# Kernel optimization log

Measured on AMD Instinct MI355X. Metric: run time of the kernel, lower is better.

## Reference

```python
import jax, jax.numpy as jnp
import numpy as np

B, S, T, K = 96, 4, 16, 36           # groups, fixed 4 slots, max tags per slot, num boxes
V_DIM, Q_DIM, H = 1024, 512, 512


def setup_inputs() -> dict:
    key = jax.random.key(0)
    k_v, k_q, k_m, k_w1, k_b1, k_w2, k_b2 = jax.random.split(key, 7)

    # deterministic ragged lengths in [1, T], cyclic -> sum is exact
    lengths = (np.arange(B * S) % T) + 1              # [B*S], sum = 24 * 136 = 3264
    N = int(lengths.sum())                            # total rows in v / q
    # binary tag-attention mask: first `len` positions set per slot
    tags_attention = (np.arange(T)[None, :] < lengths[:, None]).astype(np.int32)
    tags_attention = jnp.asarray(tags_attention.reshape(B, S, T))

    v = jax.random.normal(k_v, (N, K, V_DIM), dtype=jnp.float32)
    q = jax.random.normal(k_q, (N, Q_DIM), dtype=jnp.float32)

    # box mask: random 0/1 but guarantee at least one valid box per group
    box_mask = (jax.random.uniform(k_m, (B, K)) < 0.9).astype(jnp.float32)
    box_mask = box_mask.at[:, 0].set(1.0)

    # FCNet (weight-normed Linear + ReLU; dropout inactive at eval) and scoring Linear
    w1 = jax.random.normal(k_w1, (V_DIM + Q_DIM, H), dtype=jnp.float32) * 0.02
    b1 = jax.random.normal(k_b1, (H,), dtype=jnp.float32) * 0.02
    w2 = jax.random.normal(k_w2, (H,), dtype=jnp.float32) * 0.02
    b2 = jax.random.normal(k_b2, (), dtype=jnp.float32) * 0.02

    return {"v": v, "q": q, "box_mask": box_mask, "tags_attention": tags_attention,
            "w1": w1, "b1": b1, "w2": w2, "b2": b2}


def reference(v, q, box_mask, tags_attention, w1, b1, w2, b2):
    N, Kb, _ = v.shape
    # logits: concat(v, q repeated over boxes) -> ReLU FC -> scalar score per box
    vq = jnp.concatenate([v, jnp.broadcast_to(q[:, None, :], (N, Kb, q.shape[-1]))], axis=-1)
    joint = jax.nn.relu(jnp.einsum('nkd,dh->nkh', vq, w1) + b1)      # [N, K, H]
    logits = jnp.einsum('nkh,h->nk', joint, w2) + b2                 # [N, K]

    # pad_sequence: ragged rows -> [B, S, T, K] via vectorized gather
    Bg, Sg, Tg = tags_attention.shape
    lengths = tags_attention.sum(-1).reshape(-1)                     # [B*S]
    starts = jnp.cumsum(lengths) - lengths                           # exclusive cumsum
    idx = starts[:, None] + jnp.arange(Tg)                           # [B*S, T]
    valid = jnp.arange(Tg)[None, :] < lengths[:, None]               # [B*S, T]
    gathered = jnp.take(logits, jnp.clip(idx, 0, N - 1), axis=0)     # [B*S, T, K]
    padded = jnp.where(valid[..., None], gathered, 0.0).reshape(Bg, Sg, Tg, Kb)

    # masked_softmax (allennlp-style) over the box dim with box_mask [B,1,1,K]
    mask = box_mask[:, None, None, :]
    s = jax.nn.softmax(padded * mask, axis=-1) * mask
    w = s / (s.sum(axis=-1, keepdims=True) + 1e-13)
    return w
```

## Files before the change

kernel.cpp:

```cpp
#include <hip/hip_runtime.h>
#include <hip/hip_bf16.h>
#include <cstdint>
#include <cstddef>

#define BB 96
#define SS 4
#define TT 16
#define KK 36
#define VDIM 1024
#define QDIM 512
#define HH 512
#define W1R 1536
#define NROWS 3264
#define MM (NROWS * KK)

typedef __attribute__((ext_vector_type(8))) short short8;
typedef __attribute__((ext_vector_type(4))) float f32x4;

static __device__ __forceinline__ unsigned short f2bf(float f) {
    union { float f; unsigned u; } v; v.f = f;
    unsigned u = v.u;
    u += 0x7FFFu + ((u >> 16) & 1u);
    return (unsigned short)(u >> 16);
}

static __device__ __forceinline__ unsigned pk2(float lo, float hi) {
    __hip_bfloat162 h = __float22bfloat162_rn(make_float2(lo, hi));
    union { __hip_bfloat162 h; unsigned u; } cv;
    cv.h = h;
    return cv.u;
}

__device__ __forceinline__ void gload_lds16(const void* g, void* l) {
    __builtin_amdgcn_global_load_lds(
        (const __attribute__((address_space(1))) unsigned int*)g,
        (__attribute__((address_space(3))) unsigned int*)l, 16, 0, 0);
}

#define SB() __builtin_amdgcn_sched_barrier(0)

__global__ __launch_bounds__(256) void prep_w1T(const float* __restrict__ w1,
                                                unsigned short* __restrict__ w1T) {
    int k = blockIdx.x * 256 + threadIdx.x;
    int c = blockIdx.y;
    w1T[(size_t)c * W1R + k] = f2bf(w1[(size_t)k * HH + c]);
}

__global__ __launch_bounds__(512) void starts_kernel(const int* __restrict__ tags,
                                                     int* __restrict__ starts,
                                                     int* __restrict__ lengths) {
    __shared__ int sl[BB * SS];
    int tid = threadIdx.x;
    int len = 0;
    if (tid < BB * SS) {
#pragma unroll
        for (int i = 0; i < TT; ++i) len += tags[tid * TT + i];
        sl[tid] = len;
    }
    __syncthreads();
    for (int off = 1; off < BB * SS; off <<= 1) {
        int v = 0;
        if (tid < BB * SS && tid >= off) v = sl[tid - off];
        __syncthreads();
        if (tid < BB * SS) sl[tid] += v;
        __syncthreads();
    }
    if (tid < BB * SS) { starts[tid] = sl[tid] - len; lengths[tid] = len; }
}

__global__ __launch_bounds__(256, 3) void qproj_mfma(const float* __restrict__ q,
                                                     const unsigned short* __restrict__ w1T,
                                                     const float* __restrict__ b1,
                                                     float* __restrict__ qp) {
    __shared__ __align__(16) unsigned short At[2][64 * 64];
    __shared__ __align__(16) unsigned short Bt[2][128 * 64];

    int tid = threadIdx.x, lane = tid & 63, wid = tid >> 6;
    int wm = wid >> 1, wn = wid & 1;
    int bx = blockIdx.x;
    int nb = bx & 3, mb = bx >> 2;
    int n0q = mb * 64, cb = nb * 128;
    int lr = lane & 15, lg = lane >> 4;

    const float* a_base = q + (size_t)(n0q + wid * 16 + (lane >> 4)) * QDIM + (lane & 15) * 4;
    const unsigned short* b_base = w1T + (size_t)(cb + wid * 32 + (lane >> 3)) * W1R + 1024
                                 + (((lane & 7) ^ (lane >> 3)) * 8);

    f32x4 acc[2][4];
#pragma unroll
    for (int mt = 0; mt < 2; ++mt)
#pragma unroll
        for (int nt = 0; nt < 4; ++nt) acc[mt][nt] = (f32x4){0.f, 0.f, 0.f, 0.f};

#define QP_CVT_WRITE(DST, AR)                                                  \
    _Pragma("unroll") for (int p = 0; p < 4; ++p) {                            \
        int r = wid * 16 + (lane >> 4) + p * 4;                                \
        int boff = r * 128 + ((((lane & 15) * 8)) ^ ((r & 7) << 4));           \
        uint2 d;                                                               \
        d.x = pk2(AR[p].x, AR[p].y);                                           \
        d.y = pk2(AR[p].z, AR[p].w);                                           \
        *(uint2*)((char*)(DST) + boff) = d;                                    \
    }

#define QP_COMPUTE(AC, BC)                                                     \
    _Pragma("unroll") for (int kk = 0; kk < 2; ++kk) {                         \
        short8 af[2], bf[4];                                                   \
        _Pragma("unroll") for (int mt = 0; mt < 2; ++mt) {                     \
            int R = wm * 32 + mt * 16 + lr;                                    \
            int off = R * 128 + ((kk * 64 + lg * 16) ^ ((R & 7) << 4));        \
            af[mt] = *(const short8*)((const char*)(AC) + off);                \
        }                                                                      \
        _Pragma("unroll") for (int nt = 0; nt < 4; ++nt) {                     \
            int R = wn * 64 + nt * 16 + lr;                                    \
            int off = R * 128 + ((kk * 64 + lg * 16) ^ ((R & 7) << 4));        \
            bf[nt] = *(const short8*)((const char*)(BC) + off);                \
        }                                                                      \
        __builtin_amdgcn_s_setprio(1);                                         \
        _Pragma("unroll") for (int mt = 0; mt < 2; ++mt)                       \
            _Pragma("unroll") for (int nt = 0; nt < 4; ++nt)                   \
                acc[mt][nt] = __builtin_amdgcn_mfma_f32_16x16x32_bf16(         \
                    af[mt], bf[nt], acc[mt][nt], 0, 0, 0);                     \
        __builtin_amdgcn_s_setprio(0);                                         \
    }

    {
        float4 ar[4];
#pragma unroll
        for (int p = 0; p < 4; ++p) ar[p] = *(const float4*)(a_base + (size_t)p * 4 * QDIM);
#pragma unroll
        for (int o = 0; o < 4; ++o)
            gload_lds16(b_base + (size_t)o * 8 * W1R, &Bt[0][(wid * 32 + o * 8) * 64]);
        SB();
        QP_CVT_WRITE(&At[0][0], ar)
    }
#pragma unroll 1
    for (int t = 0; t < 7; ++t) {
        int k0 = (t + 1) * 64;
        const unsigned short* Ac = &At[t & 1][0];
        const unsigned short* Bc = &Bt[t & 1][0];
        unsigned short* An = &At[(t + 1) & 1][0];
        unsigned short* Bn = &Bt[(t + 1) & 1][0];
        float4 ar[4];
#pragma unroll
        for (int p = 0; p < 4; ++p)
            ar[p] = *(const float4*)(a_base + (size_t)p * 4 * QDIM + k0);
#pragma unroll
        for (int o = 0; o < 4; ++o)
            gload_lds16(b_base + (size_t)o * 8 * W1R + k0, &Bn[(wid * 32 + o * 8) * 64]);
        SB();
        asm volatile("s_waitcnt vmcnt(8)" ::: "memory");
        asm volatile("s_waitcnt lgkmcnt(0)" ::: "memory");
        __builtin_amdgcn_s_barrier();
        SB();
        QP_COMPUTE(Ac, Bc)
        SB();
        QP_CVT_WRITE(An, ar)
    }
    SB();
    asm volatile("s_waitcnt vmcnt(0)" ::: "memory");
    asm volatile("s_waitcnt lgkmcnt(0)" ::: "memory");
    __builtin_amdgcn_s_barrier();
    SB();
    QP_COMPUTE(&At[1][0], &Bt[1][0])
#undef QP_COMPUTE
#undef QP_CVT_WRITE

#pragma unroll
    for (int nt = 0; nt < 4; ++nt) {
        int c = cb + wn * 64 + nt * 16 + lr;
        float b1v = b1[c];
#pragma unroll
        for (int mt = 0; mt < 2; ++mt)
#pragma unroll
            for (int r = 0; r < 4; ++r) {
                int row = wm * 32 + mt * 16 + lg * 4 + r;
                qp[(size_t)(n0q + row) * HH + c] = acc[mt][nt][r] + b1v;
            }
    }
}

__global__ __launch_bounds__(256, 3) void main_gemm(const float* __restrict__ v,
                                                    const unsigned short* __restrict__ w1T,
                                                    const float* __restrict__ qp,
                                                    const float* __restrict__ w2,
                                                    float* __restrict__ logits4) {
    __shared__ __align__(16) unsigned short At[128 * 64];
    __shared__ __align__(16) unsigned short Bt[2][128 * 64];

    int tid = threadIdx.x, lane = tid & 63, wid = tid >> 6;
    int wm = wid >> 1, wn = wid & 1;
    int bx = blockIdx.x;
    int orig = (bx & 7) * 459 + (bx >> 3);
    int nb = orig & 3, mb = orig >> 2;
    int m0 = mb * 128, cb = nb * 128;
    int lr = lane & 15, lg = lane >> 4;

    const float* a_base = v + (size_t)(m0 + wid * 32 + (lane >> 4)) * VDIM + (lane & 15) * 4;
    const unsigned short* b_base = w1T + (size_t)(cb + wid * 32 + (lane >> 3)) * W1R
                                 + (((lane & 7) ^ (lane >> 3)) * 8);

    f32x4 acc[4][4];
#pragma unroll
    for (int mt = 0; mt < 4; ++mt)
#pragma unroll
        for (int nt = 0; nt < 4; ++nt) acc[mt][nt] = (f32x4){0.f, 0.f, 0.f, 0.f};

#define MG_CVT_WRITE(AR)                                                       \
    _Pragma("unroll") for (int p = 0; p < 8; ++p) {                            \
        int r = wid * 32 + (lane >> 4) + p * 4;                                \
        int boff = r * 128 + ((((lane & 15) * 8)) ^ ((r & 7) << 4));           \
        uint2 d;                                                               \
        d.x = pk2(AR[p].x, AR[p].y);                                           \
        d.y = pk2(AR[p].z, AR[p].w);                                           \
        *(uint2*)((char*)&At[0] + boff) = d;                                   \
    }

#define MG_READ_A(AF, KKC)                                                     \
    _Pragma("unroll") for (int mt = 0; mt < 4; ++mt) {                         \
        int R = wm * 64 + mt * 16 + lr;                                        \
        int off = R * 128 + (((KKC) * 64 + lg * 16) ^ ((R & 7) << 4));         \
        AF[mt] = *(const short8*)((const char*)&At[0] + off);                  \
    }

#define MG_READ_B(BF, BC, KKC)                                                 \
    _Pragma("unroll") for (int nt = 0; nt < 4; ++nt) {                         \
        int R = wn * 64 + nt * 16 + lr;                                        \
        int off = R * 128 + (((KKC) * 64 + lg * 16) ^ ((R & 7) << 4));         \
        BF[nt] = *(const short8*)((const char*)(BC) + off);                    \
    }

#define MG_MFMA(AF, BF)                                                        \
    __builtin_amdgcn_s_setprio(1);                                             \
    _Pragma("unroll") for (int mt = 0; mt < 4; ++mt)                           \
        _Pragma("unroll") for (int nt = 0; nt < 4; ++nt)                       \
            acc[mt][nt] = __builtin_amdgcn_mfma_f32_16x16x32_bf16(             \
                AF[mt], BF[nt], acc[mt][nt], 0, 0, 0);                         \
    __builtin_amdgcn_s_setprio(0);

    {
#pragma unroll
        for (int o = 0; o < 4; ++o)
            gload_lds16(b_base + (size_t)o * 8 * W1R, &Bt[0][(wid * 32 + o * 8) * 64]);
        float4 ar[8];
#pragma unroll
        for (int p = 0; p < 8; ++p) ar[p] = *(const float4*)(a_base + (size_t)p * 4 * VDIM);
        SB();
        MG_CVT_WRITE(ar)
    }

#pragma unroll 1
    for (int t = 0; t < 16; ++t) {
        int kA = (t < 15) ? (t + 1) * 64 : 960;
        const unsigned short* Bc = &Bt[t & 1][0];
        unsigned short* Bn = &Bt[(t + 1) & 1][0];
        float4 ar[8];
#pragma unroll
        for (int p = 0; p < 8; ++p)
            ar[p] = *(const float4*)(a_base + (size_t)p * 4 * VDIM + kA);
        SB();
        asm volatile("s_waitcnt vmcnt(8)" ::: "memory");
        asm volatile("s_waitcnt lgkmcnt(0)" ::: "memory");
        __builtin_amdgcn_s_barrier();
        SB();
        if (t < 15) {
#pragma unroll
            for (int o = 0; o < 4; ++o)
                gload_lds16(b_base + (size_t)o * 8 * W1R + kA, Bn + (wid * 32 + o * 8) * 64);
        }
        SB();
        {
            short8 af0[4], bf0[4];
            MG_READ_A(af0, 0)
            MG_READ_B(bf0, Bc, 0)
            MG_MFMA(af0, bf0)
        }
        {
            short8 af1[4], bf1[4];
            MG_READ_A(af1, 1)
            MG_READ_B(bf1, Bc, 1)
            MG_MFMA(af1, bf1)
        }
        SB();
        asm volatile("s_waitcnt lgkmcnt(0)" ::: "memory");
        __builtin_amdgcn_s_barrier();
        SB();
        if (t < 15) { MG_CVT_WRITE(ar) }
    }
#undef MG_MFMA
#undef MG_READ_A
#undef MG_READ_B
#undef MG_CVT_WRITE

    __syncthreads();
    float* qs = (float*)&At[0];
    float* fl = qs + 5 * 128;
    int n0 = m0 / KK;
    for (int i = tid; i < 5 * 128; i += 256) {
        int nn = n0 + (i >> 7);
        if (nn >= NROWS) nn = NROWS - 1;
        qs[i] = qp[(size_t)nn * HH + cb + (i & 127)];
    }
    __syncthreads();

    float part[4][4] = {{0.f}};
#pragma unroll
    for (int nt = 0; nt < 4; ++nt) {
        int c = wn * 64 + nt * 16 + lr;
        float w2v = w2[cb + c];
#pragma unroll
        for (int mt = 0; mt < 4; ++mt)
#pragma unroll
            for (int r = 0; r < 4; ++r) {
                int row = wm * 64 + mt * 16 + lg * 4 + r;
                int ni = (m0 + row) / KK - n0;
                float pre = acc[mt][nt][r] + qs[ni * 128 + c];
                part[mt][r] += fmaxf(pre, 0.f) * w2v;
            }
    }
#pragma unroll
    for (int mt = 0; mt < 4; ++mt)
#pragma unroll
        for (int r = 0; r < 4; ++r) {
            float s = part[mt][r];
            s += __shfl_xor(s, 1, 64);
            s += __shfl_xor(s, 2, 64);
            s += __shfl_xor(s, 4, 64);
            s += __shfl_xor(s, 8, 64);
            if (lr == 0) fl[wn * 128 + wm * 64 + mt * 16 + lg * 4 + r] = s;
        }
    __syncthreads();
    if (tid < 128)
        logits4[(size_t)nb * MM + m0 + tid] = fl[tid] + fl[128 + tid];
}

__global__ __launch_bounds__(256) void softmax_kernel(const float* __restrict__ logits4,
                                                      const float* __restrict__ box_mask,
                                                      const int* __restrict__ starts,
                                                      const int* __restrict__ lengths,
                                                      float* __restrict__ out) {
    int lane = threadIdx.x & 63;
    int g = blockIdx.x * 4 + (threadIdx.x >> 6);
    int t   = g & (TT - 1);
    int row = g >> 4;
    int b   = row >> 2;

    int length = lengths[row];
    int start  = starts[row];

    int k = lane;
    bool kv = k < KK;
    float mval = kv ? box_mask[b * KK + k] : 0.f;
    bool act = kv && (mval != 0.f);

    float l = 0.f;
    if (act && t < length) {
        size_t idx = (size_t)(start + t) * KK + k;
        l = logits4[idx] + logits4[MM + idx] + logits4[2 * (size_t)MM + idx]
          + logits4[3 * (size_t)MM + idx];
    }

    float lm = act ? l : -1e30f;
#pragma unroll
    for (int off = 32; off >= 1; off >>= 1) lm = fmaxf(lm, __shfl_xor(lm, off, 64));

    float e = act ? expf(l - lm) : 0.f;
    float se = e;
#pragma unroll
    for (int off = 32; off >= 1; off >>= 1) se += __shfl_xor(se, off, 64);

    if (kv) out[(size_t)g * KK + k] = e / se;
}

extern "C" void kernel_launch(void* const* d_in, const int* in_sizes, int n_in,
                              void* d_out, int out_size, void* d_ws, size_t ws_size,
                              hipStream_t stream) {
    const float* v        = (const float*)d_in[0];
    const float* q        = (const float*)d_in[1];
    const float* box_mask = (const float*)d_in[2];
    const int*   tags     = (const int*)d_in[3];
    const float* w1       = (const float*)d_in[4];
    const float* b1       = (const float*)d_in[5];
    const float* w2       = (const float*)d_in[6];

    char* ws = (char*)d_ws;
    unsigned short* w1T   = (unsigned short*)ws;
    float* qp      = (float*)(ws + 1572864);
    float* logits4 = (float*)(ws + 1572864 + 6684672);
    int*   starts  = (int*)(ws + 1572864 + 6684672 + 1880064);
    int*   lengths = (int*)(ws + 1572864 + 6684672 + 1880064 + 1536);
    float* out     = (float*)d_out;

    hipLaunchKernelGGL(prep_w1T, dim3(6, 512), dim3(256), 0, stream, w1, w1T);
    hipLaunchKernelGGL(starts_kernel, dim3(1), dim3(512), 0, stream, tags, starts, lengths);
    hipLaunchKernelGGL(qproj_mfma, dim3((NROWS / 64) * 4), dim3(256), 0, stream,
                       q, w1T, b1, qp);
    hipLaunchKernelGGL(main_gemm, dim3((MM / 128) * 4), dim3(256), 0, stream,
                       v, w1T, qp, w2, logits4);
    hipLaunchKernelGGL(softmax_kernel, dim3((BB * SS * TT) / 4), dim3(256), 0, stream,
                       logits4, box_mask, starts, lengths, out);
}
```

Measured before the change: 233.2 us.

## Widen main GEMM tile to 128x256 with 512-thread blocks

Changes the main fused GEMM block tile from 128x128 with 4 waves to 128x256 with 8 waves, so each block covers half of H instead of a quarter. Each converted fp32 A tile of v is reused across twice as many output columns, halving the number of times v is read from global memory and converted to bf16. The B buffer in LDS grows, the partial-logit buffer shrinks from four slices to two, and the softmax kernel sums two partials. XCD-aware block remapping is adjusted for the new grid size. Larger blocks may reduce occupancy and raise LDS pressure.

```diff
diff --git a/kernel.cpp b/kernel.cpp
--- a/kernel.cpp
+++ b/kernel.cpp
@@ -179,23 +179,25 @@
     }
 }
 
-__global__ __launch_bounds__(256, 3) void main_gemm(const float* __restrict__ v,
+__global__ __launch_bounds__(512, 4) void main_gemm(const float* __restrict__ v,
                                                     const unsigned short* __restrict__ w1T,
                                                     const float* __restrict__ qp,
                                                     const float* __restrict__ w2,
-                                                    float* __restrict__ logits4) {
+                                                    float* __restrict__ logits2) {
     __shared__ __align__(16) unsigned short At[128 * 64];
-    __shared__ __align__(16) unsigned short Bt[2][128 * 64];
+    __shared__ __align__(16) unsigned short Bt[2][256 * 64];
 
     int tid = threadIdx.x, lane = tid & 63, wid = tid >> 6;
-    int wm = wid >> 1, wn = wid & 1;
+    int wm = wid >> 2, wn = wid & 3;
     int bx = blockIdx.x;
-    int orig = (bx & 7) * 459 + (bx >> 3);
-    int nb = orig & 3, mb = orig >> 2;
-    int m0 = mb * 128, cb = nb * 128;
+    int xcd = bx & 7;
+    int base = (xcd < 4) ? xcd * 230 : 920 + (xcd - 4) * 229;
+    int orig = base + (bx >> 3);
+    int ch = orig & 1, mb = orig >> 1;
+    int m0 = mb * 128, cb = ch * 256;
     int lr = lane & 15, lg = lane >> 4;
 
-    const float* a_base = v + (size_t)(m0 + wid * 32 + (lane >> 4)) * VDIM + (lane & 15) * 4;
+    const float* a_base = v + (size_t)(m0 + wid * 16 + (lane >> 2)) * VDIM + (lane & 3) * 4;
     const unsigned short* b_base = w1T + (size_t)(cb + wid * 32 + (lane >> 3)) * W1R
                                  + (((lane & 7) ^ (lane >> 3)) * 8);
 
@@ -206,9 +208,9 @@
         for (int nt = 0; nt < 4; ++nt) acc[mt][nt] = (f32x4){0.f, 0.f, 0.f, 0.f};
 
 #define MG_CVT_WRITE(AR)                                                       \
-    _Pragma("unroll") for (int p = 0; p < 8; ++p) {                            \
-        int r = wid * 32 + (lane >> 4) + p * 4;                                \
-        int boff = r * 128 + ((((lane & 15) * 8)) ^ ((r & 7) << 4));           \
+    _Pragma("unroll") for (int p = 0; p < 4; ++p) {                            \
+        int r = wid * 16 + (lane >> 2);                                        \
+        int boff = r * 128 + (((p * 32) + (lane & 3) * 8) ^ ((r & 7) << 4));   \
         uint2 d;                                                               \
         d.x = pk2(AR[p].x, AR[p].y);                                           \
         d.y = pk2(AR[p].z, AR[p].w);                                           \
@@ -224,8 +226,8 @@
 
 #define MG_READ_B(BF, BC, KKC)                                                 \
     _Pragma("unroll") for (int nt = 0; nt < 4; ++nt) {                         \
-        int R = wn * 64 + nt * 16 + lr;                                        \
-        int off = R * 128 + (((KKC) * 64 + lg * 16) ^ ((R & 7) << 4));         \
+        int C = wn * 64 + nt * 16 + lr;                                        \
+        int off = C * 128 + (((KKC) * 64 + lg * 16) ^ ((C & 7) << 4));         \
         BF[nt] = *(const short8*)((const char*)(BC) + off);                    \
     }
 
@@ -241,9 +243,9 @@
 #pragma unroll
         for (int o = 0; o < 4; ++o)
             gload_lds16(b_base + (size_t)o * 8 * W1R, &Bt[0][(wid * 32 + o * 8) * 64]);
-        float4 ar[8];
-#pragma unroll
-        for (int p = 0; p < 8; ++p) ar[p] = *(const float4*)(a_base + (size_t)p * 4 * VDIM);
+        float4 ar[4];
+#pragma unroll
+        for (int p = 0; p < 4; ++p) ar[p] = *(const float4*)(a_base + p * 16);
         SB();
         MG_CVT_WRITE(ar)
     }
@@ -253,12 +255,12 @@
         int kA = (t < 15) ? (t + 1) * 64 : 960;
         const unsigned short* Bc = &Bt[t & 1][0];
         unsigned short* Bn = &Bt[(t + 1) & 1][0];
-        float4 ar[8];
-#pragma unroll
-        for (int p = 0; p < 8; ++p)
-            ar[p] = *(const float4*)(a_base + (size_t)p * 4 * VDIM + kA);
-        SB();
-        asm volatile("s_waitcnt vmcnt(8)" ::: "memory");
+        float4 ar[4];
+#pragma unroll
+        for (int p = 0; p < 4; ++p)
+            ar[p] = *(const float4*)(a_base + kA + p * 16);
+        SB();
+        asm volatile("s_waitcnt vmcnt(4)" ::: "memory");
         asm volatile("s_waitcnt lgkmcnt(0)" ::: "memory");
         __builtin_amdgcn_s_barrier();
         SB();
@@ -293,12 +295,12 @@
 
     __syncthreads();
     float* qs = (float*)&At[0];
-    float* fl = qs + 5 * 128;
+    float* fl = qs + 5 * 256;
     int n0 = m0 / KK;
-    for (int i = tid; i < 5 * 128; i += 256) {
-        int nn = n0 + (i >> 7);
+    for (int i = tid; i < 5 * 256; i += 512) {
+        int nn = n0 + (i >> 8);
         if (nn >= NROWS) nn = NROWS - 1;
-        qs[i] = qp[(size_t)nn * HH + cb + (i & 127)];
+        qs[i] = qp[(size_t)nn * HH + cb + (i & 255)];
     }
     __syncthreads();
 
@@ -313,7 +315,7 @@
             for (int r = 0; r < 4; ++r) {
                 int row = wm * 64 + mt * 16 + lg * 4 + r;
                 int ni = (m0 + row) / KK - n0;
-                float pre = acc[mt][nt][r] + qs[ni * 128 + c];
+                float pre = acc[mt][nt][r] + qs[ni * 256 + c];
                 part[mt][r] += fmaxf(pre, 0.f) * w2v;
             }
     }
@@ -330,10 +332,11 @@
         }
     __syncthreads();
     if (tid < 128)
-        logits4[(size_t)nb * MM + m0 + tid] = fl[tid] + fl[128 + tid];
-}
-
-__global__ __launch_bounds__(256) void softmax_kernel(const float* __restrict__ logits4,
+        logits2[(size_t)ch * MM + m0 + tid] =
+            fl[tid] + fl[128 + tid] + fl[256 + tid] + fl[384 + tid];
+}
+
+__global__ __launch_bounds__(256) void softmax_kernel(const float* __restrict__ logits2,
                                                       const float* __restrict__ box_mask,
                                                       const int* __restrict__ starts,
                                                       const int* __restrict__ lengths,
@@ -355,8 +358,7 @@
     float l = 0.f;
     if (act && t < length) {
         size_t idx = (size_t)(start + t) * KK + k;
-        l = logits4[idx] + logits4[MM + idx] + logits4[2 * (size_t)MM + idx]
-          + logits4[3 * (size_t)MM + idx];
+        l = logits2[idx] + logits2[MM + idx];
     }
 
     float lm = act ? l : -1e30f;
@@ -385,17 +387,17 @@
     char* ws = (char*)d_ws;
     unsigned short* w1T   = (unsigned short*)ws;
     float* qp      = (float*)(ws + 1572864);
-    float* logits4 = (float*)(ws + 1572864 + 6684672);
-    int*   starts  = (int*)(ws + 1572864 + 6684672 + 1880064);
-    int*   lengths = (int*)(ws + 1572864 + 6684672 + 1880064 + 1536);
+    float* logits2 = (float*)(ws + 1572864 + 6684672);
+    int*   starts  = (int*)(ws + 1572864 + 6684672 + 940032);
+    int*   lengths = (int*)(ws + 1572864 + 6684672 + 940032 + 1536);
     float* out     = (float*)d_out;
 
     hipLaunchKernelGGL(prep_w1T, dim3(6, 512), dim3(256), 0, stream, w1, w1T);
     hipLaunchKernelGGL(starts_kernel, dim3(1), dim3(512), 0, stream, tags, starts, lengths);
     hipLaunchKernelGGL(qproj_mfma, dim3((NROWS / 64) * 4), dim3(256), 0, stream,
                        q, w1T, b1, qp);
-    hipLaunchKernelGGL(main_gemm, dim3((MM / 128) * 4), dim3(256), 0, stream,
-                       v, w1T, qp, w2, logits4);
+    hipLaunchKernelGGL(main_gemm, dim3((MM / 128) * 2), dim3(512), 0, stream,
+                       v, w1T, qp, w2, logits2);
     hipLaunchKernelGGL(softmax_kernel, dim3((BB * SS * TT) / 4), dim3(256), 0, stream,
-                       logits4, box_mask, starts, lengths, out);
-}
+                       logits2, box_mask, starts, lengths, out);
+}
```

After: 263.6 us. 13.1% more time.
